# Optimization experiments

Measured on AMD Instinct MI355X. Metric: run time of the kernel, lower is better.

Reference implementation:

```python
import jax, jax.numpy as jnp
import numpy as np

# Matches MMD_loss(bandwidths=[1,2,5,10,20])
BANDWIDTHS = np.array([1.0, 2.0, 5.0, 10.0, 20.0], dtype=np.float64)
GAMMAS = (1.0 / (2.0 * BANDWIDTHS ** 2)).astype(np.float32)  # per original forward

N1, N2, D = 4096, 4096, 256


def setup_inputs() -> dict:
    key = jax.random.key(0)
    k1, k2 = jax.random.split(key)
    x1 = jax.random.normal(k1, (N1, D), dtype=jnp.float32)
    x2 = jax.random.normal(k2, (N2, D), dtype=jnp.float32)
    return {"x1": x1, "x2": x2}


def _sqdist(a, b):
    # ||a_i - b_j||^2 via GEMM identity; computed ONCE instead of per-bandwidth.
    an = jnp.sum(a * a, axis=1)  # [Na]
    bn = jnp.sum(b * b, axis=1)  # [Nb]
    d = an[:, None] + bn[None, :] - 2.0 * (a @ b.T)  # [Na, Nb]
    return jnp.maximum(d, 0.0)


def reference(x1, x2):
    d1 = x1.shape[1]
    d2 = x2.shape[1]
    s1 = jnp.float32(np.sqrt(d1))
    s2 = jnp.float32(np.sqrt(d2))

    D11 = _sqdist(x1, x1)  # [N1, N1]
    D22 = _sqdist(x2, x2)  # [N2, N2]
    D12 = _sqdist(x1, x2)  # [N1, N2]

    nb = jnp.float32(len(GAMMAS))
    m11 = jnp.float32(0.0)
    m22 = jnp.float32(0.0)
    m12 = jnp.float32(0.0)
    # small fixed loop over bandwidths; fused exp + mean per bandwidth
    for g in GAMMAS:
        g = jnp.float32(g)
        m11 = m11 + jnp.mean(jnp.exp(-(s1 * g) * D11))
        m22 = m22 + jnp.mean(jnp.exp(-(s2 * g) * D22))
        m12 = m12 + jnp.mean(jnp.exp(-(s1 * g) * D12))  # original uses d1 here too
    m11, m22, m12 = m11 / nb, m22 / nb, m12 / nb
    return jnp.sqrt(m11 - 2.0 * m12 + m22)
```

## Files before the change

kernel.cpp:

```cpp
#include <hip/hip_runtime.h>
#include <stdint.h>

typedef __attribute__((ext_vector_type(8))) short short8;
typedef __attribute__((ext_vector_type(4))) float f32x4;

#define N_ROWS 4096
#define D_DIM  256
#define NT     8192
#define TILE   128
#define NTILE  64

__device__ __forceinline__ unsigned short f2bf(float f) {
  unsigned int u = __float_as_uint(f);
  u += 0x7fffu + ((u >> 16) & 1u);
  return (unsigned short)(u >> 16);
}

__device__ __forceinline__ void gload_lds16(const void* g, void* l) {
  __builtin_amdgcn_global_load_lds(
      (const __attribute__((address_space(1))) unsigned int*)g,
      (__attribute__((address_space(3))) unsigned int*)l, 16, 0, 0);
}

__global__ __launch_bounds__(256) void mmd_prep(
    const float* __restrict__ x1, const float* __restrict__ x2,
    unsigned short* __restrict__ Zb, float* __restrict__ norms) {
  const int t = threadIdx.x, w = t >> 6, l = t & 63;
  const int r = blockIdx.x * 4 + w;
  const float* src = (r < N_ROWS) ? (x1 + (size_t)r * D_DIM)
                                  : (x2 + (size_t)(r - N_ROWS) * D_DIM);
  const float4 v = *(const float4*)(src + l * 4);
  float sq = v.x * v.x + v.y * v.y + v.z * v.z + v.w * v.w;
#pragma unroll
  for (int off = 32; off > 0; off >>= 1) sq += __shfl_down(sq, off);
  if (l == 0) norms[r] = sq;
  ushort4 o;
  o.x = f2bf(v.x); o.y = f2bf(v.y); o.z = f2bf(v.z); o.w = f2bf(v.w);
  *(ushort4*)(Zb + (size_t)r * D_DIM + l * 4) = o;
}

__global__ __launch_bounds__(256) void mmd_main(
    const unsigned short* __restrict__ Zb,
    const float* __restrict__ norms,
    float* __restrict__ partials) {
  const int br = blockIdx.x, bc = blockIdx.y;
  const int pidx = br * NTILE + bc;
  const int t = threadIdx.x;
  if (bc > br) { if (t == 0) partials[pidx] = 0.0f; return; }

  __shared__ __align__(16) unsigned short As[TILE][32];
  __shared__ __align__(16) unsigned short Bs[TILE][32];
  __shared__ float nrow[TILE], ncol[TILE];
  __shared__ float red[256];

  const int w = t >> 6, l = t & 63;
  if (t < TILE) nrow[t] = norms[br * TILE + t];
  else          ncol[t - TILE] = norms[bc * TILE + (t - TILE)];

  const int wr = (w >> 1) * 64, wc = (w & 1) * 64;
  const int fr = l & 15, fq = l >> 4;

  f32x4 acc[4][4];
#pragma unroll
  for (int m = 0; m < 4; ++m)
#pragma unroll
    for (int n = 0; n < 4; ++n)
      acc[m][n] = (f32x4){0.0f, 0.0f, 0.0f, 0.0f};

  for (int k0 = 0; k0 < D_DIM; k0 += 32) {
#pragma unroll
    for (int q = 0; q < 2; ++q) {
      const int obase = w * 2048 + q * 1024;
      const int o = obase + l * 16;
      const int row = o >> 6;
      const int chunk = (o >> 4) & 3;
      const unsigned short* ga =
          Zb + (size_t)(br * TILE + row) * D_DIM + k0 + chunk * 8;
      const unsigned short* gb =
          Zb + (size_t)(bc * TILE + row) * D_DIM + k0 + chunk * 8;
      gload_lds16(ga, (char*)(&As[0][0]) + obase);
      gload_lds16(gb, (char*)(&Bs[0][0]) + obase);
    }
    __syncthreads();

    short8 a[4], b[4];
#pragma unroll
    for (int m = 0; m < 4; ++m)
      a[m] = *(const short8*)(&As[wr + m * 16 + fr][fq * 8]);
#pragma unroll
    for (int n = 0; n < 4; ++n)
      b[n] = *(const short8*)(&Bs[wc + n * 16 + fr][fq * 8]);
#pragma unroll
    for (int m = 0; m < 4; ++m)
#pragma unroll
      for (int n = 0; n < 4; ++n)
        acc[m][n] = __builtin_amdgcn_mfma_f32_16x16x32_bf16(a[m], b[n],
                                                            acc[m][n], 0, 0, 0);
    __syncthreads();
  }

  float factor = ((br < 32) == (bc < 32)) ? 1.0f : -1.0f;
  if (br != bc) factor *= 2.0f;
  const bool diag = (br == bc);

  float sum = 0.0f;
#pragma unroll
  for (int m = 0; m < 4; ++m) {
#pragma unroll
    for (int n = 0; n < 4; ++n) {
#pragma unroll
      for (int r = 0; r < 4; ++r) {
        const int i = wr + m * 16 + fq * 4 + r;
        const int j = wc + n * 16 + fr;
        float d = nrow[i] + ncol[j] - 2.0f * acc[m][n][r];
        d = fmaxf(d, 0.0f);
        const float u = __expf(-0.02f * d);
        const float u2 = u * u, u4 = u2 * u2;
        const float u8 = u4 * u4, u16 = u8 * u8;
        const float u32v = u16 * u16, u64v = u32v * u32v;
        const float u100 = u64v * u32v * u4;
        const float u200 = u100 * u100, u400 = u200 * u200;
        float S = u + u4 + u16 + u100 + u400;
        if (diag && i == j) S = 0.0f;
        sum += S;
      }
    }
  }
  sum *= factor;

  red[t] = sum;
  __syncthreads();
#pragma unroll
  for (int k = 128; k > 0; k >>= 1) {
    if (t < k) red[t] += red[t + k];
    __syncthreads();
  }
  if (t == 0) partials[pidx] = red[0];
}

__global__ __launch_bounds__(256) void mmd_finish(
    const float* __restrict__ partials, float* __restrict__ out) {
  __shared__ float red[256];
  const int t = threadIdx.x;
  float s = 0.0f;
  for (int i = t; i < NTILE * NTILE; i += 256) s += partials[i];
  red[t] = s;
  __syncthreads();
#pragma unroll
  for (int k = 128; k > 0; k >>= 1) {
    if (t < k) red[t] += red[t + k];
    __syncthreads();
  }
  if (t == 0) {
    const float total = red[0] + 40960.0f;
    out[0] = sqrtf(fmaxf(total, 0.0f) / 83886080.0f);
  }
}

extern "C" void kernel_launch(void* const* d_in, const int* in_sizes, int n_in,
                              void* d_out, int out_size, void* d_ws, size_t ws_size,
                              hipStream_t stream) {
  const float* x1 = (const float*)d_in[0];
  const float* x2 = (const float*)d_in[1];
  unsigned short* Zb = (unsigned short*)d_ws;
  float* norms = (float*)((char*)d_ws + (size_t)NT * D_DIM * 2);
  float* partials = norms + NT;
  float* out = (float*)d_out;

  mmd_prep<<<dim3(NT / 4), dim3(256), 0, stream>>>(x1, x2, Zb, norms);
  mmd_main<<<dim3(NTILE, NTILE), dim3(256), 0, stream>>>(Zb, norms, partials);
  mmd_finish<<<dim3(1), dim3(256), 0, stream>>>(partials, out);
}
```

Before: 61.29 us.

## Load MFMA operands directly from global with register double-buffering, triangular grid

Drops the LDS staging of the A/B tiles. Each wave now loads its bf16 fragments straight from global memory into registers, alternating between two register sets so the next K-slice loads while MFMAs run on the current one, and the per-iteration __syncthreads go away. The grid is remapped to launch only the lower-triangular tile pairs, with the row and column recovered by a sqrt-based index inversion. Norms are read straight into registers instead of shared memory. The cost is that reuse across waves moves from LDS to the L1/L2 caches, with more redundant global traffic and higher register pressure.

```diff
diff --git a/kernel.cpp b/kernel.cpp
--- a/kernel.cpp
+++ b/kernel.cpp
@@ -9,17 +9,12 @@
 #define NT     8192
 #define TILE   128
 #define NTILE  64
+#define NBLK   (NTILE * (NTILE + 1) / 2)
 
 __device__ __forceinline__ unsigned short f2bf(float f) {
   unsigned int u = __float_as_uint(f);
   u += 0x7fffu + ((u >> 16) & 1u);
   return (unsigned short)(u >> 16);
-}
-
-__device__ __forceinline__ void gload_lds16(const void* g, void* l) {
-  __builtin_amdgcn_global_load_lds(
-      (const __attribute__((address_space(1))) unsigned int*)g,
-      (__attribute__((address_space(3))) unsigned int*)l, 16, 0, 0);
 }
 
 __global__ __launch_bounds__(256) void mmd_prep(
@@ -43,22 +38,25 @@
     const unsigned short* __restrict__ Zb,
     const float* __restrict__ norms,
     float* __restrict__ partials) {
-  const int br = blockIdx.x, bc = blockIdx.y;
-  const int pidx = br * NTILE + bc;
+  const int p = blockIdx.x;
+  int br = (int)((sqrtf(8.0f * (float)p + 1.0f) - 1.0f) * 0.5f);
+  while ((br + 1) * (br + 2) / 2 <= p) ++br;
+  while (br * (br + 1) / 2 > p) --br;
+  const int bc = p - br * (br + 1) / 2;
+
   const int t = threadIdx.x;
-  if (bc > br) { if (t == 0) partials[pidx] = 0.0f; return; }
-
-  __shared__ __align__(16) unsigned short As[TILE][32];
-  __shared__ __align__(16) unsigned short Bs[TILE][32];
-  __shared__ float nrow[TILE], ncol[TILE];
-  __shared__ float red[256];
-
   const int w = t >> 6, l = t & 63;
-  if (t < TILE) nrow[t] = norms[br * TILE + t];
-  else          ncol[t - TILE] = norms[bc * TILE + (t - TILE)];
-
   const int wr = (w >> 1) * 64, wc = (w & 1) * 64;
   const int fr = l & 15, fq = l >> 4;
+
+  const unsigned short* pa[4];
+  const unsigned short* pb[4];
+#pragma unroll
+  for (int m = 0; m < 4; ++m)
+    pa[m] = Zb + (size_t)(br * TILE + wr + m * 16 + fr) * D_DIM + fq * 8;
+#pragma unroll
+  for (int n = 0; n < 4; ++n)
+    pb[n] = Zb + (size_t)(bc * TILE + wc + n * 16 + fr) * D_DIM + fq * 8;
 
   f32x4 acc[4][4];
 #pragma unroll
@@ -67,37 +65,51 @@
     for (int n = 0; n < 4; ++n)
       acc[m][n] = (f32x4){0.0f, 0.0f, 0.0f, 0.0f};
 
-  for (int k0 = 0; k0 < D_DIM; k0 += 32) {
+  short8 aP[4], bP[4], aQ[4], bQ[4];
+
+#define LOADK(A, B, K)                                            \
+  do {                                                            \
+    _Pragma("unroll") for (int m = 0; m < 4; ++m)                 \
+        (A)[m] = *(const short8*)(pa[m] + (K) * 32);              \
+    _Pragma("unroll") for (int n = 0; n < 4; ++n)                 \
+        (B)[n] = *(const short8*)(pb[n] + (K) * 32);              \
+  } while (0)
+
+#define MFMAK(A, B)                                               \
+  do {                                                            \
+    _Pragma("unroll") for (int m = 0; m < 4; ++m)                 \
+        _Pragma("unroll") for (int n = 0; n < 4; ++n)             \
+            acc[m][n] = __builtin_amdgcn_mfma_f32_16x16x32_bf16(  \
+                (A)[m], (B)[n], acc[m][n], 0, 0, 0);              \
+  } while (0)
+
+  LOADK(aP, bP, 0);
+  LOADK(aQ, bQ, 1);
+  MFMAK(aP, bP);
+  LOADK(aP, bP, 2);
+  MFMAK(aQ, bQ);
+  LOADK(aQ, bQ, 3);
+  MFMAK(aP, bP);
+  LOADK(aP, bP, 4);
+  MFMAK(aQ, bQ);
+  LOADK(aQ, bQ, 5);
+  MFMAK(aP, bP);
+  LOADK(aP, bP, 6);
+  MFMAK(aQ, bQ);
+  LOADK(aQ, bQ, 7);
+  MFMAK(aP, bP);
+  MFMAK(aQ, bQ);
+
+  float nr[16];
 #pragma unroll
-    for (int q = 0; q < 2; ++q) {
-      const int obase = w * 2048 + q * 1024;
-      const int o = obase + l * 16;
-      const int row = o >> 6;
-      const int chunk = (o >> 4) & 3;
-      const unsigned short* ga =
-          Zb + (size_t)(br * TILE + row) * D_DIM + k0 + chunk * 8;
-      const unsigned short* gb =
-          Zb + (size_t)(bc * TILE + row) * D_DIM + k0 + chunk * 8;
-      gload_lds16(ga, (char*)(&As[0][0]) + obase);
-      gload_lds16(gb, (char*)(&Bs[0][0]) + obase);
-    }
-    __syncthreads();
-
-    short8 a[4], b[4];
+  for (int m = 0; m < 4; ++m)
 #pragma unroll
-    for (int m = 0; m < 4; ++m)
-      a[m] = *(const short8*)(&As[wr + m * 16 + fr][fq * 8]);
+    for (int r = 0; r < 4; ++r)
+      nr[m * 4 + r] = norms[br * TILE + wr + m * 16 + fq * 4 + r];
+  float nc[4];
 #pragma unroll
-    for (int n = 0; n < 4; ++n)
-      b[n] = *(const short8*)(&Bs[wc + n * 16 + fr][fq * 8]);
-#pragma unroll
-    for (int m = 0; m < 4; ++m)
-#pragma unroll
-      for (int n = 0; n < 4; ++n)
-        acc[m][n] = __builtin_amdgcn_mfma_f32_16x16x32_bf16(a[m], b[n],
-                                                            acc[m][n], 0, 0, 0);
-    __syncthreads();
-  }
+  for (int n = 0; n < 4; ++n)
+    nc[n] = norms[bc * TILE + wc + n * 16 + fr];
 
   float factor = ((br < 32) == (bc < 32)) ? 1.0f : -1.0f;
   if (br != bc) factor *= 2.0f;
@@ -112,7 +124,7 @@
       for (int r = 0; r < 4; ++r) {
         const int i = wr + m * 16 + fq * 4 + r;
         const int j = wc + n * 16 + fr;
-        float d = nrow[i] + ncol[j] - 2.0f * acc[m][n][r];
+        float d = nr[m * 4 + r] + nc[n] - 2.0f * acc[m][n][r];
         d = fmaxf(d, 0.0f);
         const float u = __expf(-0.02f * d);
         const float u2 = u * u, u4 = u2 * u2;
@@ -128,6 +140,7 @@
   }
   sum *= factor;
 
+  __shared__ float red[256];
   red[t] = sum;
   __syncthreads();
 #pragma unroll
@@ -135,7 +148,7 @@
     if (t < k) red[t] += red[t + k];
     __syncthreads();
   }
-  if (t == 0) partials[pidx] = red[0];
+  if (t == 0) partials[p] = red[0];
 }
 
 __global__ __launch_bounds__(256) void mmd_finish(
@@ -143,7 +156,7 @@
   __shared__ float red[256];
   const int t = threadIdx.x;
   float s = 0.0f;
-  for (int i = t; i < NTILE * NTILE; i += 256) s += partials[i];
+  for (int i = t; i < NBLK; i += 256) s += partials[i];
   red[t] = s;
   __syncthreads();
 #pragma unroll
@@ -168,6 +181,6 @@
   float* out = (float*)d_out;
 
   mmd_prep<<<dim3(NT / 4), dim3(256), 0, stream>>>(x1, x2, Zb, norms);
-  mmd_main<<<dim3(NTILE, NTILE), dim3(256), 0, stream>>>(Zb, norms, partials);
+  mmd_main<<<dim3(NBLK), dim3(256), 0, stream>>>(Zb, norms, partials);
   mmd_finish<<<dim3(1), dim3(256), 0, stream>>>(partials, out);
 }
```

New measurement: 95.41 us. 55.7% more time.
